# Performance work log

Hardware: AMD Instinct MI355X
Metric: run time of the kernel (lower is better)

Reference implementation:

```python
import jax, jax.numpy as jnp
import numpy as np

B, N, E, H, HID = 4, 2048, 1024, 16, 4096
D = E // H
EPS = 1e-5


def setup_inputs() -> dict:
    key = jax.random.key(0)
    ks = jax.random.split(key, 8)
    s = 0.02
    return {
        "x": jax.random.normal(ks[0], (B, N, E), dtype=jnp.float32),
        "Wqkv": jax.random.normal(ks[1], (3 * E, E), dtype=jnp.float32) * s,
        "bqkv": jnp.zeros((3 * E,), dtype=jnp.float32),
        "Wo": jax.random.normal(ks[2], (E, E), dtype=jnp.float32) * s,
        "bo": jnp.zeros((E,), dtype=jnp.float32),
        "ln1_g": jnp.ones((E,), dtype=jnp.float32),
        "ln1_b": jnp.zeros((E,), dtype=jnp.float32),
        "W1": jax.random.normal(ks[3], (HID, E), dtype=jnp.float32) * s,
        "bf1": jnp.zeros((HID,), dtype=jnp.float32),
        "W2": jax.random.normal(ks[4], (E, HID), dtype=jnp.float32) * s,
        "bf2": jnp.zeros((E,), dtype=jnp.float32),
        "ln2_g": jnp.ones((E,), dtype=jnp.float32),
        "ln2_b": jnp.zeros((E,), dtype=jnp.float32),
    }


def _layernorm(x, g, b):
    m = jnp.mean(x, axis=-1, keepdims=True)
    v = jnp.mean(jnp.square(x - m), axis=-1, keepdims=True)
    return (x - m) * jax.lax.rsqrt(v + EPS) * g + b


def reference(x, Wqkv, bqkv, Wo, bo, ln1_g, ln1_b, W1, bf1, W2, bf2, ln2_g, ln2_b):
    Bx, Nx, Ex = x.shape
    # --- MultiHeadSelfAttention (faithful to original, including its einsum-label quirk) ---
    qkv = x @ Wqkv.T + bqkv                                   # (B,N,3E)
    qkv = qkv.reshape(Bx, Nx, 3, H, D).transpose(2, 0, 3, 1, 4)  # (3,B,H,N,D)
    q, k, v = qkv[0], qkv[1], qkv[2]                          # each (B,H,N,D)
    # original torch labels: q/k interpreted as (n,q,h,d) -> energy (B,N,H,H)
    energy = jnp.einsum('nqhd,nkhd->nhqk', q, k)
    attention = jax.nn.softmax(energy / (Ex ** 0.5), axis=-1)  # softmax over heads axis
    out = jnp.einsum('nhql,nlhd->nqhd', attention, v).reshape(Bx, Nx, Ex)
    attn_out = out @ Wo.T + bo
    # --- residual + LN1 ---
    h = _layernorm(x + attn_out, ln1_g, ln1_b)
    # --- FFN (dropout is identity in eval) ---
    f = jax.nn.gelu(h @ W1.T + bf1, approximate=False) @ W2.T + bf2
    # --- residual + LN2 ---
    return _layernorm(h + f, ln2_g, ln2_b)
```

## Files before the change

kernel.cpp:

```cpp
#include <hip/hip_runtime.h>
#include <hip/hip_bf16.h>
#include <math.h>

typedef __hip_bfloat16 bf16;
typedef __bf16 bf8v __attribute__((ext_vector_type(8)));
typedef float f4v __attribute__((ext_vector_type(4)));

__device__ inline float gelu_act(float v) {
    return 0.5f * v * (1.f + erff(v * 0.70710678118654752f));
}

__device__ inline void gld16(const void* g, void* l) {
    __builtin_amdgcn_global_load_lds(
        (__attribute__((address_space(1))) void*)g,
        (__attribute__((address_space(3))) void*)l, 16, 0, 0);
}

__global__ __launch_bounds__(256)
void cast_f2b(const float* __restrict__ X, bf16* __restrict__ Y, long n)
{
    const long i = ((long)blockIdx.x * 256 + threadIdx.x) * 4;
    if (i + 3 < n) {
        const float4 v = *(const float4*)(X + i);
        Y[i + 0] = __float2bfloat16(v.x);
        Y[i + 1] = __float2bfloat16(v.y);
        Y[i + 2] = __float2bfloat16(v.z);
        Y[i + 3] = __float2bfloat16(v.w);
    }
}

template<int ACT, bool HASRES, typename CT, int K>
__global__ __launch_bounds__(256, 4)
void gemm128(const bf16* __restrict__ A, const bf16* __restrict__ W,
             const float* __restrict__ bias, const float* __restrict__ Rr,
             CT* __restrict__ C, int N)
{
    extern __shared__ __align__(16) unsigned short lds[];
    constexpr int NT   = K / 32;
    constexpr int SLOT = 8192;

    const int o     = blockIdx.y * gridDim.x + blockIdx.x;
    const int local = o >> 3;
    const int bm  = (o & 7) * 8 + (local & 7);
    const int bn  = local >> 3;
    const long row0 = (long)bm * 128;
    const long col0 = (long)bn * 128;

    const int tid  = threadIdx.x;
    const int lane = tid & 63;
    const int wave = tid >> 6;
    const int wm = wave >> 1;
    const int wn = wave & 1;
    const int fr = lane & 15;
    const int ksw = (((lane >> 4) ^ ((lane >> 1) & 3)) << 3);

    const int srow = tid >> 2;
    const int csrc = (tid & 3) ^ ((srow >> 1) & 3);
    const unsigned short* gA = (const unsigned short*)A + (row0 + srow) * (long)K + csrc * 8;
    const unsigned short* gB = (const unsigned short*)W + (col0 + srow) * (long)K + csrc * 8;
    const int woff = wave * 512;

    auto stage = [&](int t) {
        const long k0 = (long)t * 32;
        unsigned short* sl = lds + (t & 1) * SLOT + woff;
        gld16(gA + k0,                 sl);
        gld16(gA + 64 * (long)K + k0,  sl + 2048);
        gld16(gB + k0,                 sl + 4096);
        gld16(gB + 64 * (long)K + k0,  sl + 6144);
    };

    f4v acc[4][4];
#pragma unroll
    for (int i = 0; i < 4; ++i)
#pragma unroll
        for (int j = 0; j < 4; ++j) acc[i][j] = {0.f, 0.f, 0.f, 0.f};

    stage(0);
    __syncthreads();

#pragma unroll 2
    for (int t = 0; t < NT; ++t) {
        if (t + 1 < NT) stage(t + 1);

        const unsigned short* sA = lds + (t & 1) * SLOT;
        const unsigned short* sB = sA + 4096;

        bf8v afrag[4], bfrag[4];
#pragma unroll
        for (int x = 0; x < 4; ++x) {
            afrag[x] = *(const bf8v*)&sA[(wm * 64 + x * 16 + fr) * 32 + ksw];
            bfrag[x] = *(const bf8v*)&sB[(wn * 64 + x * 16 + fr) * 32 + ksw];
        }
#pragma unroll
        for (int mi = 0; mi < 4; ++mi)
#pragma unroll
            for (int ni = 0; ni < 4; ++ni)
                acc[mi][ni] = __builtin_amdgcn_mfma_f32_16x16x32_bf16(
                    afrag[mi], bfrag[ni], acc[mi][ni], 0, 0, 0);

        __syncthreads();
    }

    constexpr int STR = 132;
    float* eb = (float*)lds;
    const int q4    = (lane >> 4) * 4;
    const int lcol  = (tid & 31) * 4;
    const long nbase = col0 + lcol;
    const float4 b4 = *(const float4*)&bias[nbase];
    const float bb[4] = {b4.x, b4.y, b4.z, b4.w};

#pragma unroll
    for (int h = 0; h < 2; ++h) {
        if (h) __syncthreads();
        if (wm == h) {
#pragma unroll
            for (int mi = 0; mi < 4; ++mi)
#pragma unroll
                for (int ni = 0; ni < 4; ++ni)
#pragma unroll
                    for (int r = 0; r < 4; ++r)
                        eb[(mi * 16 + q4 + r) * STR + wn * 64 + ni * 16 + fr] = acc[mi][ni][r];
        }
        __syncthreads();
#pragma unroll
        for (int i = 0; i < 8; ++i) {
            const int  rh = i * 8 + (tid >> 5);
            const long gr = row0 + h * 64 + rh;
            const f4v v = *(const f4v*)&eb[rh * STR + lcol];
            float ov[4];
#pragma unroll
            for (int c = 0; c < 4; ++c) ov[c] = v[c] + bb[c];
            if (HASRES) {
                const float4 r4 = *(const float4*)&Rr[gr * (long)N + nbase];
                const float ra[4] = {r4.x, r4.y, r4.z, r4.w};
#pragma unroll
                for (int c = 0; c < 4; ++c) ov[c] += ra[c];
            }
            if (ACT == 1) {
#pragma unroll
                for (int c = 0; c < 4; ++c) ov[c] = gelu_act(ov[c]);
            }
            if constexpr (sizeof(CT) == 2) {
                ushort4 s;
                bf16* sp = (bf16*)&s;
#pragma unroll
                for (int c = 0; c < 4; ++c) sp[c] = __float2bfloat16(ov[c]);
                *(ushort4*)&C[gr * (long)N + nbase] = s;
            } else {
                *(float4*)&C[gr * (long)N + nbase] = make_float4(ov[0], ov[1], ov[2], ov[3]);
            }
        }
    }
}

__global__ __launch_bounds__(256)
void attn_kernel(const bf16* __restrict__ qkv, bf16* __restrict__ scr)
{
    __shared__ float sb[4][3392];
    const int tid = threadIdx.x;
    const int wave = tid >> 6, lane = tid & 63;
    const int m = blockIdx.x * 4 + wave;

    float* q = sb[wave];
    float* k = q + 1040;
    float* v = k + 1040;
    float* a = v + 1040;

    const bf16* rowp = qkv + (size_t)m * 3072;
    for (int i = lane; i < 1024; i += 64) {
        int hh = i >> 6, dd = i & 63;
        q[hh * 65 + dd] = __bfloat162float(rowp[i]);
        k[hh * 65 + dd] = __bfloat162float(rowp[1024 + i]);
        v[hh * 65 + dd] = __bfloat162float(rowp[2048 + i]);
    }
    __syncthreads();

    const int h1 = lane & 15, qd = lane >> 4;
    float e[4];
#pragma unroll
    for (int j = 0; j < 4; ++j) {
        const float* qr = q + h1 * 65;
        const float* kr = k + (qd * 4 + j) * 65;
        float s0 = 0.f;
        for (int d = 0; d < 64; ++d) s0 += qr[d] * kr[d];
        e[j] = s0 * 0.03125f;
    }
    float mx = fmaxf(fmaxf(e[0], e[1]), fmaxf(e[2], e[3]));
    mx = fmaxf(mx, __shfl_xor(mx, 16, 64));
    mx = fmaxf(mx, __shfl_xor(mx, 32, 64));
    float p[4], ps = 0.f;
#pragma unroll
    for (int j = 0; j < 4; ++j) { p[j] = expf(e[j] - mx); ps += p[j]; }
    ps += __shfl_xor(ps, 16, 64);
    ps += __shfl_xor(ps, 32, 64);
    const float inv = 1.f / ps;
#pragma unroll
    for (int j = 0; j < 4; ++j) a[h1 * 17 + qd * 4 + j] = p[j] * inv;
    __syncthreads();

    const int h = lane & 15, dg = lane >> 4;
    float arow[16];
#pragma unroll
    for (int l2 = 0; l2 < 16; ++l2) arow[l2] = a[h * 17 + l2];
    const int b = m >> 11, j = m & 2047;
    bf16* op = scr + (((size_t)b * 2048 + h * 128 + (j >> 4)) * 1024 + (j & 15) * 64);
    for (int t = 0; t < 16; ++t) {
        const int d = dg * 16 + t;
        float o = 0.f;
#pragma unroll
        for (int l2 = 0; l2 < 16; ++l2) o += arow[l2] * v[l2 * 65 + d];
        op[d] = __float2bfloat16(o);
    }
}

__global__ __launch_bounds__(256)
void ln_kernel(const float* __restrict__ X, const float* __restrict__ G,
               const float* __restrict__ Bt, float* __restrict__ Y32,
               bf16* __restrict__ Yb)
{
    __shared__ float rs[4], rq[4];
    const int tid = threadIdx.x;
    const long row = blockIdx.x;
    const float* xp = X + row * 1024;
    float x[4];
#pragma unroll
    for (int i = 0; i < 4; ++i) x[i] = xp[tid + 256 * i];

    float s = x[0] + x[1] + x[2] + x[3];
#pragma unroll
    for (int off = 32; off; off >>= 1) s += __shfl_down(s, off, 64);
    if ((tid & 63) == 0) rs[tid >> 6] = s;
    __syncthreads();
    const float mean = (rs[0] + rs[1] + rs[2] + rs[3]) * (1.f / 1024.f);

    float qv = 0.f;
#pragma unroll
    for (int i = 0; i < 4; ++i) { float d = x[i] - mean; qv += d * d; }
#pragma unroll
    for (int off = 32; off; off >>= 1) qv += __shfl_down(qv, off, 64);
    if ((tid & 63) == 0) rq[tid >> 6] = qv;
    __syncthreads();
    const float var = (rq[0] + rq[1] + rq[2] + rq[3]) * (1.f / 1024.f);
    const float rstd = rsqrtf(var + 1e-5f);

#pragma unroll
    for (int i = 0; i < 4; ++i) {
        const int e = tid + 256 * i;
        const float yv = (x[i] - mean) * rstd * G[e] + Bt[e];
        Y32[row * 1024 + e] = yv;
        if (Yb) Yb[row * 1024 + e] = __float2bfloat16(yv);
    }
}

extern "C" void kernel_launch(void* const* d_in, const int* in_sizes, int n_in,
                              void* d_out, int out_size, void* d_ws, size_t ws_size,
                              hipStream_t stream)
{
    (void)in_sizes; (void)n_in; (void)out_size;
    const float* x    = (const float*)d_in[0];
    const float* Wqkv = (const float*)d_in[1];
    const float* bqkv = (const float*)d_in[2];
    const float* Wo   = (const float*)d_in[3];
    const float* bo   = (const float*)d_in[4];
    const float* g1   = (const float*)d_in[5];
    const float* b1   = (const float*)d_in[6];
    const float* W1   = (const float*)d_in[7];
    const float* bf1  = (const float*)d_in[8];
    const float* W2   = (const float*)d_in[9];
    const float* bf2  = (const float*)d_in[10];
    const float* g2   = (const float*)d_in[11];
    const float* b2   = (const float*)d_in[12];
    float* out = (float*)d_out;

    if (ws_size < 125829120ULL) return;

    char* ws = (char*)d_ws;
    bf16* qkv   = (bf16*)(ws + 0);
    float* t    = (float*)(ws + 0);
    bf16* u     = (bf16*)(ws + 0);
    bf16* Wqkvb = (bf16*)(ws + 67108864);
    bf16* Wob   = (bf16*)(ws + 73400320);
    bf16* W1b   = (bf16*)(ws + 75497472);
    bf16* W2b   = (bf16*)(ws + 83886080);
    bf16* xb    = (bf16*)(ws + 92274688);
    bf16* scr   = (bf16*)(ws + 92274688);
    bf16* hb    = (bf16*)(ws + 109051904);
    float* h    = out;

    constexpr unsigned LDS_SZ = 33792;

    cast_f2b<<<8192, 256, 0, stream>>>(x,    xb,    8388608);
    cast_f2b<<<3072, 256, 0, stream>>>(Wqkv, Wqkvb, 3145728);
    cast_f2b<<<1024, 256, 0, stream>>>(Wo,   Wob,   1048576);
    cast_f2b<<<4096, 256, 0, stream>>>(W1,   W1b,   4194304);
    cast_f2b<<<4096, 256, 0, stream>>>(W2,   W2b,   4194304);

    gemm128<0, false, bf16, 1024><<<dim3(64, 24), 256, LDS_SZ, stream>>>(xb, Wqkvb, bqkv, nullptr, qkv, 3072);
    attn_kernel<<<2048, 256, 0, stream>>>(qkv, scr);
    gemm128<0, true, float, 1024><<<dim3(64, 8), 256, LDS_SZ, stream>>>(scr, Wob, bo, x, t, 1024);
    ln_kernel<<<8192, 256, 0, stream>>>(t, g1, b1, h, hb);
    gemm128<1, false, bf16, 1024><<<dim3(64, 32), 256, LDS_SZ, stream>>>(hb, W1b, bf1, nullptr, u, 4096);
    gemm128<0, true, float, 4096><<<dim3(64, 8), 256, LDS_SZ, stream>>>(u, W2b, bf2, h, out, 1024);
    ln_kernel<<<8192, 256, 0, stream>>>(out, g2, b2, out, nullptr);
}
```

Before: 463.4 us.

## Add 256x128-tile GEMM kernel for QKV and FFN1 projections

Introduces gemm_wide, a GEMM variant with 256x128 output tiles (each wave computes 128x64 via 8x4 MFMA accumulators) and its own block swizzle and staged epilogue through LDS. It is used for the QKV projection and the first FFN GEMM, which have wide N. The larger tile raises arithmetic intensity and halves A/B reloads per output, at the cost of more registers, larger LDS (48KB) and lower occupancy (launch bound 3), plus fewer blocks in flight.

```diff
diff --git a/kernel.cpp b/kernel.cpp
--- a/kernel.cpp
+++ b/kernel.cpp
@@ -26,6 +26,138 @@
         Y[i + 1] = __float2bfloat16(v.y);
         Y[i + 2] = __float2bfloat16(v.z);
         Y[i + 3] = __float2bfloat16(v.w);
+    }
+}
+
+template<int ACT, bool HASRES, typename CT, int K>
+__global__ __launch_bounds__(256, 3)
+void gemm_wide(const bf16* __restrict__ A, const bf16* __restrict__ W,
+               const float* __restrict__ bias, const float* __restrict__ Rr,
+               CT* __restrict__ C, int N)
+{
+    extern __shared__ __align__(16) unsigned short lds[];
+    constexpr int NT   = K / 32;
+    constexpr int SLOT = 12288;
+
+    const int o     = blockIdx.y * 32 + blockIdx.x;
+    const int local = o >> 3;
+    const int bm = (o & 7) * 4 + (local & 3);
+    const int bn = local >> 2;
+    const long row0 = (long)bm * 256;
+    const long col0 = (long)bn * 128;
+
+    const int tid  = threadIdx.x;
+    const int lane = tid & 63;
+    const int wave = tid >> 6;
+    const int wm = wave >> 1;
+    const int wn = wave & 1;
+    const int fr = lane & 15;
+    const int ksw = (((lane >> 4) ^ ((lane >> 1) & 3)) << 3);
+
+    const int srow = tid >> 2;
+    const int csrc = (tid & 3) ^ ((srow >> 1) & 3);
+    const unsigned short* gA = (const unsigned short*)A + (row0 + srow) * (long)K + csrc * 8;
+    const unsigned short* gB = (const unsigned short*)W + (col0 + srow) * (long)K + csrc * 8;
+    const int woff = wave * 512;
+
+    auto stage = [&](int t) {
+        const long k0 = (long)t * 32;
+        unsigned short* sl = lds + (t & 1) * SLOT + woff;
+        gld16(gA + k0,                  sl);
+        gld16(gA +  64 * (long)K + k0,  sl + 2048);
+        gld16(gA + 128 * (long)K + k0,  sl + 4096);
+        gld16(gA + 192 * (long)K + k0,  sl + 6144);
+        gld16(gB + k0,                  sl + 8192);
+        gld16(gB +  64 * (long)K + k0,  sl + 10240);
+    };
+
+    f4v acc[8][4];
+#pragma unroll
+    for (int i = 0; i < 8; ++i)
+#pragma unroll
+        for (int j = 0; j < 4; ++j) acc[i][j] = {0.f, 0.f, 0.f, 0.f};
+
+    stage(0);
+    __syncthreads();
+
+#pragma unroll 2
+    for (int t = 0; t < NT; ++t) {
+        if (t + 1 < NT) stage(t + 1);
+
+        const unsigned short* sA = lds + (t & 1) * SLOT;
+        const unsigned short* sB = sA + 8192;
+
+        bf8v bfrag[4];
+#pragma unroll
+        for (int ni = 0; ni < 4; ++ni)
+            bfrag[ni] = *(const bf8v*)&sB[(wn * 64 + ni * 16 + fr) * 32 + ksw];
+#pragma unroll
+        for (int mh = 0; mh < 2; ++mh) {
+            bf8v afrag[4];
+#pragma unroll
+            for (int mi = 0; mi < 4; ++mi)
+                afrag[mi] = *(const bf8v*)&sA[(wm * 128 + mh * 64 + mi * 16 + fr) * 32 + ksw];
+#pragma unroll
+            for (int mi = 0; mi < 4; ++mi)
+#pragma unroll
+                for (int ni = 0; ni < 4; ++ni)
+                    acc[mh * 4 + mi][ni] = __builtin_amdgcn_mfma_f32_16x16x32_bf16(
+                        afrag[mi], bfrag[ni], acc[mh * 4 + mi][ni], 0, 0, 0);
+        }
+
+        __syncthreads();
+    }
+
+    constexpr int STR = 132;
+    float* eb = (float*)lds;
+    const int q4   = (lane >> 4) * 4;
+    const int lcol = (tid & 31) * 4;
+    const long nbase = col0 + lcol;
+    const float4 b4 = *(const float4*)&bias[nbase];
+    const float bb[4] = {b4.x, b4.y, b4.z, b4.w};
+
+#pragma unroll
+    for (int c = 0; c < 4; ++c) {
+        if (c) __syncthreads();
+        if (wm == (c >> 1)) {
+            const int mb = (c & 1) * 4;
+#pragma unroll
+            for (int mi = 0; mi < 4; ++mi)
+#pragma unroll
+                for (int ni = 0; ni < 4; ++ni)
+#pragma unroll
+                    for (int r = 0; r < 4; ++r)
+                        eb[(mi * 16 + q4 + r) * STR + wn * 64 + ni * 16 + fr] = acc[mb + mi][ni][r];
+        }
+        __syncthreads();
+#pragma unroll
+        for (int i = 0; i < 8; ++i) {
+            const int  rh = i * 8 + (tid >> 5);
+            const long gr = row0 + c * 64 + rh;
+            const f4v v = *(const f4v*)&eb[rh * STR + lcol];
+            float ov[4];
+#pragma unroll
+            for (int cc = 0; cc < 4; ++cc) ov[cc] = v[cc] + bb[cc];
+            if (HASRES) {
+                const float4 r4 = *(const float4*)&Rr[gr * (long)N + nbase];
+                const float ra[4] = {r4.x, r4.y, r4.z, r4.w};
+#pragma unroll
+                for (int cc = 0; cc < 4; ++cc) ov[cc] += ra[cc];
+            }
+            if (ACT == 1) {
+#pragma unroll
+                for (int cc = 0; cc < 4; ++cc) ov[cc] = gelu_act(ov[cc]);
+            }
+            if constexpr (sizeof(CT) == 2) {
+                ushort4 s;
+                bf16* sp = (bf16*)&s;
+#pragma unroll
+                for (int cc = 0; cc < 4; ++cc) sp[cc] = __float2bfloat16(ov[cc]);
+                *(ushort4*)&C[gr * (long)N + nbase] = s;
+            } else {
+                *(float4*)&C[gr * (long)N + nbase] = make_float4(ov[0], ov[1], ov[2], ov[3]);
+            }
+        }
     }
 }
 
@@ -287,7 +419,8 @@
     bf16* hb    = (bf16*)(ws + 109051904);
     float* h    = out;
 
-    constexpr unsigned LDS_SZ = 33792;
+    constexpr unsigned LDS_128  = 33792;
+    constexpr unsigned LDS_WIDE = 49152;
 
     cast_f2b<<<8192, 256, 0, stream>>>(x,    xb,    8388608);
     cast_f2b<<<3072, 256, 0, stream>>>(Wqkv, Wqkvb, 3145728);
@@ -295,11 +428,11 @@
     cast_f2b<<<4096, 256, 0, stream>>>(W1,   W1b,   4194304);
     cast_f2b<<<4096, 256, 0, stream>>>(W2,   W2b,   4194304);
 
-    gemm128<0, false, bf16, 1024><<<dim3(64, 24), 256, LDS_SZ, stream>>>(xb, Wqkvb, bqkv, nullptr, qkv, 3072);
+    gemm_wide<0, false, bf16, 1024><<<dim3(32, 24), 256, LDS_WIDE, stream>>>(xb, Wqkvb, bqkv, nullptr, qkv, 3072);
     attn_kernel<<<2048, 256, 0, stream>>>(qkv, scr);
-    gemm128<0, true, float, 1024><<<dim3(64, 8), 256, LDS_SZ, stream>>>(scr, Wob, bo, x, t, 1024);
+    gemm128<0, true, float, 1024><<<dim3(64, 8), 256, LDS_128, stream>>>(scr, Wob, bo, x, t, 1024);
     ln_kernel<<<8192, 256, 0, stream>>>(t, g1, b1, h, hb);
-    gemm128<1, false, bf16, 1024><<<dim3(64, 32), 256, LDS_SZ, stream>>>(hb, W1b, bf1, nullptr, u, 4096);
-    gemm128<0, true, float, 4096><<<dim3(64, 8), 256, LDS_SZ, stream>>>(u, W2b, bf2, h, out, 1024);
+    gemm_wide<1, false, bf16, 1024><<<dim3(32, 32), 256, LDS_WIDE, stream>>>(hb, W1b, bf1, nullptr, u, 4096);
+    gemm128<0, true, float, 4096><<<dim3(64, 8), 256, LDS_128, stream>>>(u, W2b, bf2, h, out, 1024);
     ln_kernel<<<8192, 256, 0, stream>>>(out, g2, b2, out, nullptr);
 }
```

Measured after the change: 469.9 us. Within noise of the previous version (+1.4%).

## Split-K the FFN down-projection with atomic accumulation and shrink epilogue LDS

Applied to the files above, without the earlier changes.

The K=4096 W2 GEMM is split into two K halves along grid z. Each half atomically adds its partial tile into the output buffer, which already holds the LN1 residual, and only the first split adds the bias. The point is to double the block count for a GEMM that previously launched only 512 tiles. Separately, the epilogue now stages 32 rows at a time instead of 64, which cuts the dynamic LDS size and raises the launch-bounds occupancy hint from 4 to 5. The trade-off is 16M scalar float atomics to global memory and a non-deterministic summation order.

```diff
diff --git a/kernel.cpp b/kernel.cpp
--- a/kernel.cpp
+++ b/kernel.cpp
@@ -29,14 +29,14 @@
     }
 }
 
-template<int ACT, bool HASRES, typename CT, int K>
-__global__ __launch_bounds__(256, 4)
+template<int EPI, bool HASRES, typename CT, int KL, int KR>
+__global__ __launch_bounds__(256, 5)
 void gemm128(const bf16* __restrict__ A, const bf16* __restrict__ W,
              const float* __restrict__ bias, const float* __restrict__ Rr,
              CT* __restrict__ C, int N)
 {
     extern __shared__ __align__(16) unsigned short lds[];
-    constexpr int NT   = K / 32;
+    constexpr int NT   = KL / 32;
     constexpr int SLOT = 8192;
 
     const int o     = blockIdx.y * gridDim.x + blockIdx.x;
@@ -45,6 +45,7 @@
     const int bn  = local >> 3;
     const long row0 = (long)bm * 128;
     const long col0 = (long)bn * 128;
+    const long koff = (long)blockIdx.z * KL;
 
     const int tid  = threadIdx.x;
     const int lane = tid & 63;
@@ -52,21 +53,22 @@
     const int wm = wave >> 1;
     const int wn = wave & 1;
     const int fr = lane & 15;
+    const int q4 = (lane >> 4) * 4;
     const int ksw = (((lane >> 4) ^ ((lane >> 1) & 3)) << 3);
 
     const int srow = tid >> 2;
     const int csrc = (tid & 3) ^ ((srow >> 1) & 3);
-    const unsigned short* gA = (const unsigned short*)A + (row0 + srow) * (long)K + csrc * 8;
-    const unsigned short* gB = (const unsigned short*)W + (col0 + srow) * (long)K + csrc * 8;
+    const unsigned short* gA = (const unsigned short*)A + (row0 + srow) * (long)KR + koff + csrc * 8;
+    const unsigned short* gB = (const unsigned short*)W + (col0 + srow) * (long)KR + koff + csrc * 8;
     const int woff = wave * 512;
 
     auto stage = [&](int t) {
         const long k0 = (long)t * 32;
         unsigned short* sl = lds + (t & 1) * SLOT + woff;
-        gld16(gA + k0,                 sl);
-        gld16(gA + 64 * (long)K + k0,  sl + 2048);
-        gld16(gB + k0,                 sl + 4096);
-        gld16(gB + 64 * (long)K + k0,  sl + 6144);
+        gld16(gA + k0,                  sl);
+        gld16(gA + 64 * (long)KR + k0,  sl + 2048);
+        gld16(gB + k0,                  sl + 4096);
+        gld16(gB + 64 * (long)KR + k0,  sl + 6144);
     };
 
     f4v acc[4][4];
@@ -101,50 +103,68 @@
         __syncthreads();
     }
 
+    if constexpr (EPI == 2) {
+        const bool addb = (blockIdx.z == 0);
+#pragma unroll
+        for (int ni = 0; ni < 4; ++ni) {
+            const long n = col0 + wn * 64 + ni * 16 + fr;
+            const float bvv = addb ? bias[n] : 0.f;
+#pragma unroll
+            for (int mi = 0; mi < 4; ++mi) {
+                const long mb = row0 + wm * 64 + mi * 16 + q4;
+#pragma unroll
+                for (int r = 0; r < 4; ++r)
+                    atomicAdd((float*)&C[(mb + r) * (long)N + n], acc[mi][ni][r] + bvv);
+            }
+        }
+        return;
+    }
+
     constexpr int STR = 132;
     float* eb = (float*)lds;
-    const int q4    = (lane >> 4) * 4;
     const int lcol  = (tid & 31) * 4;
     const long nbase = col0 + lcol;
     const float4 b4 = *(const float4*)&bias[nbase];
     const float bb[4] = {b4.x, b4.y, b4.z, b4.w};
 
 #pragma unroll
-    for (int h = 0; h < 2; ++h) {
-        if (h) __syncthreads();
-        if (wm == h) {
-#pragma unroll
-            for (int mi = 0; mi < 4; ++mi)
+    for (int c = 0; c < 4; ++c) {
+        if (c) __syncthreads();
+        if (wm == (c >> 1)) {
+            const int m0 = (c & 1) * 2;
+#pragma unroll
+            for (int mi = 0; mi < 2; ++mi)
 #pragma unroll
                 for (int ni = 0; ni < 4; ++ni)
 #pragma unroll
                     for (int r = 0; r < 4; ++r)
-                        eb[(mi * 16 + q4 + r) * STR + wn * 64 + ni * 16 + fr] = acc[mi][ni][r];
+                        eb[((m0 + mi) * 16 + q4 + r - (c & 1) * 32) * STR
+                           + wn * 64 + ni * 16 + fr] = acc[m0 + mi][ni][r];
         }
         __syncthreads();
 #pragma unroll
-        for (int i = 0; i < 8; ++i) {
+        for (int i = 0; i < 4; ++i) {
             const int  rh = i * 8 + (tid >> 5);
-            const long gr = row0 + h * 64 + rh;
+            const long gr = row0 + c * 32 + rh;
             const f4v v = *(const f4v*)&eb[rh * STR + lcol];
             float ov[4];
 #pragma unroll
-            for (int c = 0; c < 4; ++c) ov[c] = v[c] + bb[c];
+            for (int cc = 0; cc < 4; ++cc) ov[cc] = v[cc] + bb[cc];
             if (HASRES) {
                 const float4 r4 = *(const float4*)&Rr[gr * (long)N + nbase];
                 const float ra[4] = {r4.x, r4.y, r4.z, r4.w};
 #pragma unroll
-                for (int c = 0; c < 4; ++c) ov[c] += ra[c];
+                for (int cc = 0; cc < 4; ++cc) ov[cc] += ra[cc];
             }
-            if (ACT == 1) {
-#pragma unroll
-                for (int c = 0; c < 4; ++c) ov[c] = gelu_act(ov[c]);
+            if (EPI == 1) {
+#pragma unroll
+                for (int cc = 0; cc < 4; ++cc) ov[cc] = gelu_act(ov[cc]);
             }
             if constexpr (sizeof(CT) == 2) {
                 ushort4 s;
                 bf16* sp = (bf16*)&s;
 #pragma unroll
-                for (int c = 0; c < 4; ++c) sp[c] = __float2bfloat16(ov[c]);
+                for (int cc = 0; cc < 4; ++cc) sp[cc] = __float2bfloat16(ov[cc]);
                 *(ushort4*)&C[gr * (long)N + nbase] = s;
             } else {
                 *(float4*)&C[gr * (long)N + nbase] = make_float4(ov[0], ov[1], ov[2], ov[3]);
@@ -287,7 +307,7 @@
     bf16* hb    = (bf16*)(ws + 109051904);
     float* h    = out;
 
-    constexpr unsigned LDS_SZ = 33792;
+    constexpr unsigned LDS_128 = 32768;
 
     cast_f2b<<<8192, 256, 0, stream>>>(x,    xb,    8388608);
     cast_f2b<<<3072, 256, 0, stream>>>(Wqkv, Wqkvb, 3145728);
@@ -295,11 +315,11 @@
     cast_f2b<<<4096, 256, 0, stream>>>(W1,   W1b,   4194304);
     cast_f2b<<<4096, 256, 0, stream>>>(W2,   W2b,   4194304);
 
-    gemm128<0, false, bf16, 1024><<<dim3(64, 24), 256, LDS_SZ, stream>>>(xb, Wqkvb, bqkv, nullptr, qkv, 3072);
+    gemm128<0, false, bf16, 1024, 1024><<<dim3(64, 24), 256, LDS_128, stream>>>(xb, Wqkvb, bqkv, nullptr, qkv, 3072);
     attn_kernel<<<2048, 256, 0, stream>>>(qkv, scr);
-    gemm128<0, true, float, 1024><<<dim3(64, 8), 256, LDS_SZ, stream>>>(scr, Wob, bo, x, t, 1024);
+    gemm128<0, true, float, 1024, 1024><<<dim3(64, 8), 256, LDS_128, stream>>>(scr, Wob, bo, x, t, 1024);
     ln_kernel<<<8192, 256, 0, stream>>>(t, g1, b1, h, hb);
-    gemm128<1, false, bf16, 1024><<<dim3(64, 32), 256, LDS_SZ, stream>>>(hb, W1b, bf1, nullptr, u, 4096);
-    gemm128<0, true, float, 4096><<<dim3(64, 8), 256, LDS_SZ, stream>>>(u, W2b, bf2, h, out, 1024);
+    gemm128<1, false, bf16, 1024, 1024><<<dim3(64, 32), 256, LDS_128, stream>>>(hb, W1b, bf1, nullptr, u, 4096);
+    gemm128<2, false, float, 2048, 4096><<<dim3(64, 8, 2), 256, LDS_128, stream>>>(u, W2b, bf2, nullptr, out, 1024);
     ln_kernel<<<8192, 256, 0, stream>>>(out, g2, b2, out, nullptr);
 }
```

New measurement: 519.8 us. 12.2% more time.
